# Optimization experiments

Hardware: AMD Instinct MI355X
Metric: run time of the kernel (lower is better)

Reference implementation:

```python
import jax, jax.numpy as jnp
import numpy as np

N_HEADS = 16

def setup_inputs() -> dict:
    key = jax.random.key(0)
    ks = jax.random.split(key, 5)
    B, T, C = 4, 2048, 1024
    s = 0.02
    return {
        "x": jax.random.normal(ks[0], (B, T, C), jnp.float32),
        "W_attn": jax.random.normal(ks[1], (C, 3 * C), jnp.float32) * s,
        "b_attn": jax.random.normal(ks[2], (3 * C,), jnp.float32) * s,
        "W_proj": jax.random.normal(ks[3], (C, C), jnp.float32) * s,
        "b_proj": jax.random.normal(ks[4], (C,), jnp.float32) * s,
    }

def reference(x, W_attn, b_attn, W_proj, b_proj):
    B, T, C = x.shape
    H = N_HEADS
    D = C // H  # head dim
    qkv = x @ W_attn + b_attn                      # [B,T,3C]
    q, k, v = jnp.split(qkv, 3, axis=2)
    # [B,T,C] -> [B,H,T,D]
    q = q.reshape(B, T, H, D).transpose(0, 2, 1, 3)
    k = k.reshape(B, T, H, D).transpose(0, 2, 1, 3)
    v = v.reshape(B, T, H, D).transpose(0, 2, 1, 3)
    scale = 1.0 / jnp.sqrt(jnp.asarray(D, q.dtype))
    attn = jnp.einsum("bhqd,bhkd->bhqk", q, k) * scale  # [B,H,T,T]
    causal = jnp.tril(jnp.ones((T, T), bool))
    attn = jnp.where(causal[None, None], attn, -jnp.inf)
    attn = jax.nn.softmax(attn, axis=-1)
    y = jnp.einsum("bhqk,bhkd->bhqd", attn, v)          # [B,H,T,D]
    y = y.transpose(0, 2, 1, 3).reshape(B, T, C)
    return y @ W_proj + b_proj
```

## Files before the change

kernel.cpp:

```cpp
#include <hip/hip_runtime.h>

typedef __bf16 bf16x8 __attribute__((ext_vector_type(8)));
typedef float f32x4 __attribute__((ext_vector_type(4)));
typedef float f32x16 __attribute__((ext_vector_type(16)));
typedef unsigned short ushort8 __attribute__((ext_vector_type(8)));
typedef unsigned int uint4v __attribute__((ext_vector_type(4)));

__device__ __forceinline__ unsigned short f2bf(float f) {
  __bf16 b = (__bf16)f;
  return __builtin_bit_cast(unsigned short, b);
}

#define GLOAD_LDS16(g, l)                                              \
  __builtin_amdgcn_global_load_lds(                                    \
      (const __attribute__((address_space(1))) void*)(g),              \
      (__attribute__((address_space(3))) void*)(l), 16, 0, 0)

__global__ __launch_bounds__(256) void f32_to_bf16_kernel(const float* __restrict__ in,
                                                          __bf16* __restrict__ out) {
  int i = blockIdx.x * 256 + threadIdx.x;
  const float4* p = (const float4*)(in + (size_t)i * 8);
  float4 f0 = p[0], f1 = p[1];
  ushort8 u = {f2bf(f0.x), f2bf(f0.y), f2bf(f0.z), f2bf(f0.w),
               f2bf(f1.x), f2bf(f1.y), f2bf(f1.z), f2bf(f1.w)};
  *(ushort8*)((unsigned short*)out + (size_t)i * 8) = u;
}

__global__ __launch_bounds__(256) void wtrans_kernel(const float* __restrict__ W,
                                                     __bf16* __restrict__ Wt,
                                                     int K, int N) {
  __shared__ float tile[32][33];
  int tx = threadIdx.x, ty = threadIdx.y;
  int n0 = blockIdx.x * 32, k0 = blockIdx.y * 32;
#pragma unroll
  for (int i = 0; i < 32; i += 8)
    tile[ty + i][tx] = W[(size_t)(k0 + ty + i) * N + n0 + tx];
  __syncthreads();
#pragma unroll
  for (int i = 0; i < 32; i += 8)
    Wt[(size_t)(n0 + ty + i) * K + k0 + tx] = (__bf16)tile[tx][ty + i];
}

template <int OUT_F32>
__global__ __launch_bounds__(256) void gemm_bt_kernel(const __bf16* __restrict__ Ab,
                                                      const __bf16* __restrict__ Bt,
                                                      const float* __restrict__ bias,
                                                      void* __restrict__ Cp,
                                                      int M, int N, int K) {
  __shared__ __align__(16) unsigned short As[128 * 32];
  __shared__ __align__(16) unsigned short Bs[128 * 32];
  const int tid = threadIdx.x;
  const int lane = tid & 63;
  const int wid = tid >> 6;
  const int lr = lane & 15, lg = lane >> 4;
  const int gx = gridDim.x;
  int nwg = gx * gridDim.y;
  int bid = blockIdx.y * gx + blockIdx.x;
  if ((nwg & 7) == 0) {
    int cpx = nwg >> 3;
    bid = (bid & 7) * cpx + (bid >> 3);
  }
  const int m0 = (bid / gx) * 128, n0 = (bid % gx) * 128;
  const int wm = (wid >> 1) * 64, wn = (wid & 1) * 64;
  const int sr = tid >> 2, sc = (tid & 3) * 8;
  const unsigned short* Ag = (const unsigned short*)Ab + (size_t)(m0 + sr) * K + sc;
  const unsigned short* Bg = (const unsigned short*)Bt + (size_t)(n0 + sr) * K + sc;
  f32x4 acc[4][4] = {};
  for (int k0 = 0; k0 < K; k0 += 32) {
    GLOAD_LDS16(Ag + k0, As + tid * 8);
    GLOAD_LDS16(Ag + (size_t)64 * K + k0, As + 2048 + tid * 8);
    GLOAD_LDS16(Bg + k0, Bs + tid * 8);
    GLOAD_LDS16(Bg + (size_t)64 * K + k0, Bs + 2048 + tid * 8);
    __syncthreads();
    bf16x8 af[4], bfr[4];
#pragma unroll
    for (int i = 0; i < 4; ++i) af[i] = *(const bf16x8*)&As[(wm + i * 16 + lr) * 32 + lg * 8];
#pragma unroll
    for (int i = 0; i < 4; ++i) bfr[i] = *(const bf16x8*)&Bs[(wn + i * 16 + lr) * 32 + lg * 8];
#pragma unroll
    for (int i = 0; i < 4; ++i)
#pragma unroll
      for (int jn = 0; jn < 4; ++jn)
        acc[i][jn] = __builtin_amdgcn_mfma_f32_16x16x32_bf16(af[i], bfr[jn], acc[i][jn], 0, 0, 0);
    __syncthreads();
  }
#pragma unroll
  for (int i = 0; i < 4; ++i)
#pragma unroll
    for (int jn = 0; jn < 4; ++jn)
#pragma unroll
      for (int jj = 0; jj < 4; ++jj) {
        int row = m0 + wm + i * 16 + lg * 4 + jj;
        int col = n0 + wn + jn * 16 + lr;
        float v = acc[i][jn][jj] + bias[col];
        if (OUT_F32)
          ((float*)Cp)[(size_t)row * N + col] = v;
        else
          ((unsigned short*)Cp)[(size_t)row * N + col] = f2bf(v);
      }
}

__global__ __launch_bounds__(256) void reshape_qk_kernel(const __bf16* __restrict__ qkv,
                                                         __bf16* __restrict__ Q,
                                                         __bf16* __restrict__ Ko) {
  int tid = blockIdx.x * 256 + threadIdx.x;
  int d8 = tid & 7;
  int t = (tid >> 3) & 2047;
  int h = (tid >> 14) & 15;
  int b = tid >> 18;
  size_t src = (size_t)(b * 2048 + t) * 3072 + h * 64 + d8 * 8;
  size_t dst = (size_t)((b * 16 + h) * 2048 + t) * 64 + d8 * 8;
  *(ushort8*)((unsigned short*)Q + dst) = *(const ushort8*)((const unsigned short*)qkv + src);
  *(ushort8*)((unsigned short*)Ko + dst) =
      *(const ushort8*)((const unsigned short*)qkv + src + 1024);
}

__global__ __launch_bounds__(256) void vtrans_kernel(const __bf16* __restrict__ qkv,
                                                     __bf16* __restrict__ Vt) {
  __shared__ __align__(16) unsigned short tile[64][72];
  int bh = blockIdx.y, b = bh >> 4, h = bh & 15;
  int t0 = blockIdx.x * 64;
  int tid = threadIdx.x;
#pragma unroll
  for (int p = 0; p < 2; ++p) {
    int idx = p * 256 + tid;
    int r = idx >> 3, c8 = (idx & 7) * 8;
    *(ushort8*)&tile[r][c8] = *(const ushort8*)((const unsigned short*)qkv +
                                                (size_t)(b * 2048 + t0 + r) * 3072 + 2048 +
                                                h * 64 + c8);
  }
  __syncthreads();
#pragma unroll
  for (int p = 0; p < 2; ++p) {
    int idx = p * 256 + tid;
    int d = idx >> 3, c8 = (idx & 7) * 8;
    ushort8 u;
#pragma unroll
    for (int i = 0; i < 8; ++i) u[i] = tile[c8 + i][d];
    *(ushort8*)((unsigned short*)Vt + (size_t)(bh * 64 + d) * 2048 + t0 + c8) = u;
  }
}

__global__ __launch_bounds__(256) void attn_kernel(const __bf16* __restrict__ Q,
                                                   const __bf16* __restrict__ Kg,
                                                   const __bf16* __restrict__ Vt,
                                                   __bf16* __restrict__ yb) {
  __shared__ __align__(16) unsigned short Ks[2][64][72];
  __shared__ __align__(16) unsigned short Vs[2][64][72];
  const int bx = blockIdx.x;
  const int qb = 15 - (bx >> 6);
  const int bh = bx & 63;
  const int b = bh >> 4, h = bh & 15;
  const int tid = threadIdx.x, wid = tid >> 6, lane = tid & 63;
  const int lq = lane & 31, hi = lane >> 5;
  const unsigned short* Qh = (const unsigned short*)Q + (size_t)bh * 2048 * 64;
  const unsigned short* Kh = (const unsigned short*)Kg + (size_t)bh * 2048 * 64;
  const unsigned short* Vh = (const unsigned short*)Vt + (size_t)bh * 64 * 2048;
  const int q0w = qb * 128 + wid * 32;
  const int jmax_w = 2 * qb + (wid >> 1);
  const int qrel = (wid & 1) * 32 + lq;
  const int J = 2 * qb + 2;

  bf16x8 qf[4];
#pragma unroll
  for (int dc = 0; dc < 4; ++dc)
    qf[dc] = *(const bf16x8*)(Qh + (size_t)(q0w + lq) * 64 + dc * 16 + hi * 8);

  f32x16 yacc[2] = {};
  float m_r = -1e30f, l_r = 0.f;
  const float sc = 0.125f * 1.44269504f;

  {
#pragma unroll
    for (int p = 0; p < 2; ++p) {
      int idx = p * 256 + tid;
      int r = idx >> 3, c8 = (idx & 7) * 8;
      *(ushort8*)&Ks[0][r][c8] = *(const ushort8*)(Kh + (size_t)r * 64 + c8);
      *(ushort8*)&Vs[0][r][c8] = *(const ushort8*)(Vh + (size_t)r * 2048 + c8);
    }
  }

  for (int j = 0; j < J; ++j) {
    __syncthreads();
    if (j + 1 < J) {
      int bi = (j + 1) & 1;
#pragma unroll
      for (int p = 0; p < 2; ++p) {
        int idx = p * 256 + tid;
        int r = idx >> 3, c8 = (idx & 7) * 8;
        *(ushort8*)&Ks[bi][r][c8] =
            *(const ushort8*)(Kh + (size_t)((j + 1) * 64 + r) * 64 + c8);
        *(ushort8*)&Vs[bi][r][c8] =
            *(const ushort8*)(Vh + (size_t)r * 2048 + (j + 1) * 64 + c8);
      }
    }
    if (j <= jmax_w) {
      const int cb = j & 1;
      f32x16 sa[2];
#pragma unroll
      for (int kt32 = 0; kt32 < 2; ++kt32) {
        f32x16 s = {};
#pragma unroll
        for (int dc = 0; dc < 4; ++dc) {
          bf16x8 kf = *(const bf16x8*)&Ks[cb][kt32 * 32 + lq][dc * 16 + hi * 8];
          s = __builtin_amdgcn_mfma_f32_32x32x16_bf16(kf, qf[dc], s, 0, 0, 0);
        }
        sa[kt32] = s;
      }
      float pmax = -1e30f;
#pragma unroll
      for (int kt32 = 0; kt32 < 2; ++kt32)
#pragma unroll
        for (int reg = 0; reg < 16; ++reg) {
          float v = sa[kt32][reg] * sc;
          int kl = kt32 * 32 + (reg & 3) + 8 * (reg >> 2) + 4 * hi;
          if (j == jmax_w && kl > qrel) v = -1e30f;
          sa[kt32][reg] = v;
          pmax = fmaxf(pmax, v);
        }
      pmax = fmaxf(pmax, __shfl_xor(pmax, 32));
      const bool need = __any(pmax > m_r + 8.f) != 0;
      const float mnew = need ? fmaxf(m_r, pmax) : m_r;
      const float alpha = exp2f(m_r - mnew);
      unsigned int u[2][8];
      float rs = 0.f;
#pragma unroll
      for (int kt32 = 0; kt32 < 2; ++kt32)
#pragma unroll
        for (int r = 0; r < 8; ++r) {
          float p0 = exp2f(sa[kt32][2 * r] - mnew);
          float p1 = exp2f(sa[kt32][2 * r + 1] - mnew);
          rs += p0 + p1;
          unsigned int up;
          asm("v_cvt_pk_bf16_f32 %0, %1, %2" : "=v"(up) : "v"(p0), "v"(p1));
          u[kt32][r] = up;
        }
      rs += __shfl_xor(rs, 32);
      l_r = l_r * alpha + rs;
      m_r = mnew;
      if (need) {
#pragma unroll
        for (int reg = 0; reg < 16; ++reg) {
          int row = (reg & 3) + 8 * (reg >> 2) + 4 * hi;
          float ac = __shfl(alpha, row);
          yacc[0][reg] *= ac;
          yacc[1][reg] *= ac;
        }
      }
#pragma unroll
      for (int kt = 0; kt < 4; ++kt) {
        const int kt32 = kt >> 1, off = 4 * (kt & 1);
        unsigned int a0 = u[kt32][off + 0], a2 = u[kt32][off + 2];
        unsigned int a1 = u[kt32][off + 1], a3 = u[kt32][off + 3];
        asm("v_permlane32_swap_b32 %0, %1" : "+v"(a0), "+v"(a2));
        asm("v_permlane32_swap_b32 %0, %1" : "+v"(a1), "+v"(a3));
        uint4v pav = {a0, a1, a2, a3};
        bf16x8 paf = __builtin_bit_cast(bf16x8, pav);
#pragma unroll
        for (int dt = 0; dt < 2; ++dt) {
          bf16x8 vf = *(const bf16x8*)&Vs[cb][dt * 32 + lq][kt * 16 + hi * 8];
          yacc[dt] = __builtin_amdgcn_mfma_f32_32x32x16_bf16(paf, vf, yacc[dt], 0, 0, 0);
        }
      }
    }
  }
#pragma unroll
  for (int reg = 0; reg < 16; ++reg) {
    int row = (reg & 3) + 8 * (reg >> 2) + 4 * hi;
    float linv = 1.f / __shfl(l_r, row);
    int qg = q0w + row;
#pragma unroll
    for (int dt = 0; dt < 2; ++dt) {
      float v = yacc[dt][reg] * linv;
      ((unsigned short*)yb)[(size_t)(b * 2048 + qg) * 1024 + h * 64 + dt * 32 + lq] = f2bf(v);
    }
  }
}

extern "C" void kernel_launch(void* const* d_in, const int* in_sizes, int n_in,
                              void* d_out, int out_size, void* d_ws, size_t ws_size,
                              hipStream_t stream) {
  const float* x = (const float*)d_in[0];
  const float* W_attn = (const float*)d_in[1];
  const float* b_attn = (const float*)d_in[2];
  const float* W_proj = (const float*)d_in[3];
  const float* b_proj = (const float*)d_in[4];
  float* out = (float*)d_out;
  char* ws = (char*)d_ws;

  size_t off = 0;
  __bf16* WtA = (__bf16*)(ws + off); off += (size_t)3072 * 1024 * 2;
  __bf16* WtP = (__bf16*)(ws + off); off += (size_t)1024 * 1024 * 2;
  __bf16* qkv = (__bf16*)(ws + off); off += (size_t)8192 * 3072 * 2;
  __bf16* Qb  = (__bf16*)(ws + off); off += (size_t)64 * 2048 * 64 * 2;
  __bf16* Kb  = (__bf16*)(ws + off); off += (size_t)64 * 2048 * 64 * 2;
  __bf16* Vtb = (__bf16*)(ws + off); off += (size_t)64 * 2048 * 64 * 2;
  __bf16* xyb = (__bf16*)(ws + off); off += (size_t)8192 * 1024 * 2;
  __bf16* xb = xyb;
  __bf16* yb = xyb;
  (void)ws_size; (void)in_sizes; (void)n_in; (void)out_size;

  f32_to_bf16_kernel<<<4096, 256, 0, stream>>>(x, xb);
  wtrans_kernel<<<dim3(3072 / 32, 1024 / 32), dim3(32, 8), 0, stream>>>(W_attn, WtA, 1024, 3072);
  wtrans_kernel<<<dim3(1024 / 32, 1024 / 32), dim3(32, 8), 0, stream>>>(W_proj, WtP, 1024, 1024);
  gemm_bt_kernel<0><<<dim3(24, 64), 256, 0, stream>>>(xb, WtA, b_attn, qkv, 8192, 3072, 1024);
  reshape_qk_kernel<<<4096, 256, 0, stream>>>(qkv, Qb, Kb);
  vtrans_kernel<<<dim3(32, 64), 256, 0, stream>>>(qkv, Vtb);
  attn_kernel<<<dim3(1024), 256, 0, stream>>>(Qb, Kb, Vtb, yb);
  gemm_bt_kernel<1><<<dim3(8, 64), 256, 0, stream>>>(yb, WtP, b_proj, out, 8192, 1024, 1024);
}
```

Measured before the change: 209.1 us.

## Read Q/K directly from qkv, register-prefetch tiles, prescale Q, add setprio

```diff
diff --git a/kernel.cpp b/kernel.cpp
--- a/kernel.cpp
+++ b/kernel.cpp
@@ -9,6 +9,10 @@
 __device__ __forceinline__ unsigned short f2bf(float f) {
   __bf16 b = (__bf16)f;
   return __builtin_bit_cast(unsigned short, b);
+}
+__device__ __forceinline__ float bf2f(unsigned short u) {
+  unsigned int x = ((unsigned int)u) << 16;
+  return __builtin_bit_cast(float, x);
 }
 
 #define GLOAD_LDS16(g, l)                                              \
@@ -100,21 +104,6 @@
       }
 }
 
-__global__ __launch_bounds__(256) void reshape_qk_kernel(const __bf16* __restrict__ qkv,
-                                                         __bf16* __restrict__ Q,
-                                                         __bf16* __restrict__ Ko) {
-  int tid = blockIdx.x * 256 + threadIdx.x;
-  int d8 = tid & 7;
-  int t = (tid >> 3) & 2047;
-  int h = (tid >> 14) & 15;
-  int b = tid >> 18;
-  size_t src = (size_t)(b * 2048 + t) * 3072 + h * 64 + d8 * 8;
-  size_t dst = (size_t)((b * 16 + h) * 2048 + t) * 64 + d8 * 8;
-  *(ushort8*)((unsigned short*)Q + dst) = *(const ushort8*)((const unsigned short*)qkv + src);
-  *(ushort8*)((unsigned short*)Ko + dst) =
-      *(const ushort8*)((const unsigned short*)qkv + src + 1024);
-}
-
 __global__ __launch_bounds__(256) void vtrans_kernel(const __bf16* __restrict__ qkv,
                                                      __bf16* __restrict__ Vt) {
   __shared__ __align__(16) unsigned short tile[64][72];
@@ -141,8 +130,7 @@
   }
 }
 
-__global__ __launch_bounds__(256) void attn_kernel(const __bf16* __restrict__ Q,
-                                                   const __bf16* __restrict__ Kg,
+__global__ __launch_bounds__(256) void attn_kernel(const __bf16* __restrict__ qkvp,
                                                    const __bf16* __restrict__ Vt,
                                                    __bf16* __restrict__ yb) {
   __shared__ __align__(16) unsigned short Ks[2][64][72];
@@ -153,50 +141,62 @@
   const int b = bh >> 4, h = bh & 15;
   const int tid = threadIdx.x, wid = tid >> 6, lane = tid & 63;
   const int lq = lane & 31, hi = lane >> 5;
-  const unsigned short* Qh = (const unsigned short*)Q + (size_t)bh * 2048 * 64;
-  const unsigned short* Kh = (const unsigned short*)Kg + (size_t)bh * 2048 * 64;
+  const unsigned short* qkv = (const unsigned short*)qkvp;
   const unsigned short* Vh = (const unsigned short*)Vt + (size_t)bh * 64 * 2048;
   const int q0w = qb * 128 + wid * 32;
   const int jmax_w = 2 * qb + (wid >> 1);
   const int qrel = (wid & 1) * 32 + lq;
   const int J = 2 * qb + 2;
-
+  const int r0 = tid >> 3, r1 = 32 + (tid >> 3), c8 = (tid & 7) * 8;
+  const unsigned short* Kcol = qkv + (size_t)b * 2048 * 3072 + 1024 + h * 64 + c8;
+
+  const float qs = 0.125f * 1.44269504f;
   bf16x8 qf[4];
-#pragma unroll
-  for (int dc = 0; dc < 4; ++dc)
-    qf[dc] = *(const bf16x8*)(Qh + (size_t)(q0w + lq) * 64 + dc * 16 + hi * 8);
+  {
+    const unsigned short* Qg = qkv + (size_t)(b * 2048 + q0w + lq) * 3072 + h * 64;
+#pragma unroll
+    for (int dc = 0; dc < 4; ++dc) {
+      ushort8 uq = *(const ushort8*)(Qg + dc * 16 + hi * 8);
+      uint4v w;
+#pragma unroll
+      for (int i = 0; i < 4; ++i) {
+        float lo = bf2f(uq[2 * i]) * qs;
+        float hh = bf2f(uq[2 * i + 1]) * qs;
+        unsigned int up;
+        asm("v_cvt_pk_bf16_f32 %0, %1, %2" : "=v"(up) : "v"(lo), "v"(hh));
+        w[i] = up;
+      }
+      qf[dc] = __builtin_bit_cast(bf16x8, w);
+    }
+  }
 
   f32x16 yacc[2] = {};
   float m_r = -1e30f, l_r = 0.f;
-  const float sc = 0.125f * 1.44269504f;
-
-  {
-#pragma unroll
-    for (int p = 0; p < 2; ++p) {
-      int idx = p * 256 + tid;
-      int r = idx >> 3, c8 = (idx & 7) * 8;
-      *(ushort8*)&Ks[0][r][c8] = *(const ushort8*)(Kh + (size_t)r * 64 + c8);
-      *(ushort8*)&Vs[0][r][c8] = *(const ushort8*)(Vh + (size_t)r * 2048 + c8);
-    }
-  }
+
+  ushort8 kr0, kr1, vr0, vr1;
+  auto issue_loads = [&](int jt) {
+    kr0 = *(const ushort8*)(Kcol + (size_t)(jt * 64 + r0) * 3072);
+    kr1 = *(const ushort8*)(Kcol + (size_t)(jt * 64 + r1) * 3072);
+    vr0 = *(const ushort8*)(Vh + (size_t)r0 * 2048 + jt * 64 + c8);
+    vr1 = *(const ushort8*)(Vh + (size_t)r1 * 2048 + jt * 64 + c8);
+  };
+  auto write_tile = [&](int bi) {
+    *(ushort8*)&Ks[bi][r0][c8] = kr0;
+    *(ushort8*)&Ks[bi][r1][c8] = kr1;
+    *(ushort8*)&Vs[bi][r0][c8] = vr0;
+    *(ushort8*)&Vs[bi][r1][c8] = vr1;
+  };
+
+  issue_loads(0);
+  write_tile(0);
+  if (J > 1) issue_loads(1);
 
   for (int j = 0; j < J; ++j) {
     __syncthreads();
-    if (j + 1 < J) {
-      int bi = (j + 1) & 1;
-#pragma unroll
-      for (int p = 0; p < 2; ++p) {
-        int idx = p * 256 + tid;
-        int r = idx >> 3, c8 = (idx & 7) * 8;
-        *(ushort8*)&Ks[bi][r][c8] =
-            *(const ushort8*)(Kh + (size_t)((j + 1) * 64 + r) * 64 + c8);
-        *(ushort8*)&Vs[bi][r][c8] =
-            *(const ushort8*)(Vh + (size_t)r * 2048 + (j + 1) * 64 + c8);
-      }
-    }
+    const int cb = j & 1;
     if (j <= jmax_w) {
-      const int cb = j & 1;
       f32x16 sa[2];
+      __builtin_amdgcn_s_setprio(1);
 #pragma unroll
       for (int kt32 = 0; kt32 < 2; ++kt32) {
         f32x16 s = {};
@@ -207,17 +207,23 @@
         }
         sa[kt32] = s;
       }
+      __builtin_amdgcn_s_setprio(0);
+      if (j == jmax_w) {
+#pragma unroll
+        for (int kt32 = 0; kt32 < 2; ++kt32)
+#pragma unroll
+          for (int reg = 0; reg < 16; ++reg) {
+            int kl = kt32 * 32 + (reg & 3) + 8 * (reg >> 2) + 4 * hi;
+            if (kl > qrel) sa[kt32][reg] = -1e30f;
+          }
+      }
       float pmax = -1e30f;
 #pragma unroll
       for (int kt32 = 0; kt32 < 2; ++kt32)
 #pragma unroll
-        for (int reg = 0; reg < 16; ++reg) {
-          float v = sa[kt32][reg] * sc;
-          int kl = kt32 * 32 + (reg & 3) + 8 * (reg >> 2) + 4 * hi;
-          if (j == jmax_w && kl > qrel) v = -1e30f;
-          sa[kt32][reg] = v;
-          pmax = fmaxf(pmax, v);
-        }
+        for (int reg = 0; reg < 16; reg += 4)
+          pmax = fmaxf(pmax, fmaxf(fmaxf(sa[kt32][reg], sa[kt32][reg + 1]),
+                                   fmaxf(sa[kt32][reg + 2], sa[kt32][reg + 3])));
       pmax = fmaxf(pmax, __shfl_xor(pmax, 32));
       const bool need = __any(pmax > m_r + 8.f) != 0;
       const float mnew = need ? fmaxf(m_r, pmax) : m_r;
@@ -247,6 +253,7 @@
           yacc[1][reg] *= ac;
         }
       }
+      __builtin_amdgcn_s_setprio(1);
 #pragma unroll
       for (int kt = 0; kt < 4; ++kt) {
         const int kt32 = kt >> 1, off = 4 * (kt & 1);
@@ -262,6 +269,11 @@
           yacc[dt] = __builtin_amdgcn_mfma_f32_32x32x16_bf16(paf, vf, yacc[dt], 0, 0, 0);
         }
       }
+      __builtin_amdgcn_s_setprio(0);
+    }
+    if (j + 1 < J) {
+      write_tile(cb ^ 1);
+      if (j + 2 < J) issue_loads(j + 2);
     }
   }
 #pragma unroll
@@ -292,8 +304,6 @@
   __bf16* WtA = (__bf16*)(ws + off); off += (size_t)3072 * 1024 * 2;
   __bf16* WtP = (__bf16*)(ws + off); off += (size_t)1024 * 1024 * 2;
   __bf16* qkv = (__bf16*)(ws + off); off += (size_t)8192 * 3072 * 2;
-  __bf16* Qb  = (__bf16*)(ws + off); off += (size_t)64 * 2048 * 64 * 2;
-  __bf16* Kb  = (__bf16*)(ws + off); off += (size_t)64 * 2048 * 64 * 2;
   __bf16* Vtb = (__bf16*)(ws + off); off += (size_t)64 * 2048 * 64 * 2;
   __bf16* xyb = (__bf16*)(ws + off); off += (size_t)8192 * 1024 * 2;
   __bf16* xb = xyb;
@@ -304,8 +314,7 @@
   wtrans_kernel<<<dim3(3072 / 32, 1024 / 32), dim3(32, 8), 0, stream>>>(W_attn, WtA, 1024, 3072);
   wtrans_kernel<<<dim3(1024 / 32, 1024 / 32), dim3(32, 8), 0, stream>>>(W_proj, WtP, 1024, 1024);
   gemm_bt_kernel<0><<<dim3(24, 64), 256, 0, stream>>>(xb, WtA, b_attn, qkv, 8192, 3072, 1024);
-  reshape_qk_kernel<<<4096, 256, 0, stream>>>(qkv, Qb, Kb);
   vtrans_kernel<<<dim3(32, 64), 256, 0, stream>>>(qkv, Vtb);
-  attn_kernel<<<dim3(1024), 256, 0, stream>>>(Qb, Kb, Vtb, yb);
+  attn_kernel<<<dim3(1024), 256, 0, stream>>>(qkv, Vtb, yb);
   gemm_bt_kernel<1><<<dim3(8, 64), 256, 0, stream>>>(yb, WtP, b_proj, out, 8192, 1024, 1024);
 }
```

After: 206.6 us. No clear change (-1.2%).
